# Kernel optimization log

Measured on AMD Instinct MI355X. Metric: run time of the kernel, lower is better.

Reference implementation:

```python
import jax, jax.numpy as jnp
import numpy as np

N_PTS0 = 32   # sample points per line
N_PTS1 = 8    # after 1d max-pool (kernel 4)
DIM_LOI = 128
DIM_FC = 1024
TOPK = 300
H = W = 128
L = 10000
C_FEAT = 256


def setup_inputs() -> dict:
    key = jax.random.key(0)
    ks = jax.random.split(key, 8)
    f32 = jnp.float32
    return {
        'output': jax.random.normal(ks[0], (1, 9, H, W), f32),
        'features': jax.random.normal(ks[1], (1, C_FEAT, H, W), f32),
        'lines_pred': jax.random.uniform(ks[2], (L, 4), f32, 0.0, W - 1.0),
        'fc1_w': jax.random.normal(ks[3], (DIM_LOI, C_FEAT), f32) * 0.05,
        'fc1_b': jnp.zeros((DIM_LOI,), f32),
        'w1': jax.random.normal(ks[4], (DIM_FC, DIM_LOI * N_PTS1), f32) * 0.02,
        'b1': jnp.zeros((DIM_FC,), f32),
        'w2': jax.random.normal(ks[5], (DIM_FC, DIM_FC), f32) * 0.02,
        'b2': jnp.zeros((DIM_FC,), f32),
        'w3': jax.random.normal(ks[6], (1, DIM_FC), f32) * 0.02,
        'b3': jnp.zeros((1,), f32),
    }


def _nms(a):
    # a: [H, W]; 3x3 max-pool NMS, keep only local maxima
    ap = jax.lax.reduce_window(a[None, None], -jnp.inf, jax.lax.max,
                               (1, 1, 3, 3), (1, 1, 1, 1), 'SAME')[0, 0]
    return a * (a == ap).astype(a.dtype)


def _pooling(loi, lines, w1, b1, w2, b2, w3, b3):
    # loi: [D, H, W]; lines: [L, 4]
    h, w = loi.shape[1], loi.shape[2]
    tspan = jnp.linspace(0.0, 1.0, N_PTS0)[None, None, :]          # [1,1,P]
    U, V = lines[:, :2], lines[:, 2:]
    pts = U[:, :, None] * tspan + V[:, :, None] * (1.0 - tspan) - 0.5  # [L,2,P]
    pts = jnp.transpose(pts, (0, 2, 1)).reshape(-1, 2)              # [L*P,2]
    px, py = pts[:, 0], pts[:, 1]
    px0 = jnp.clip(jnp.floor(px), 0, w - 1)
    py0 = jnp.clip(jnp.floor(py), 0, h - 1)
    px1 = jnp.clip(px0 + 1, 0, w - 1)
    py1 = jnp.clip(py0 + 1, 0, h - 1)
    ix0, iy0 = px0.astype(jnp.int32), py0.astype(jnp.int32)
    ix1, iy1 = px1.astype(jnp.int32), py1.astype(jnp.int32)
    xp = (loi[:, iy0, ix0] * (py1 - py) * (px1 - px)
          + loi[:, iy1, ix0] * (py - py0) * (px1 - px)
          + loi[:, iy0, ix1] * (py1 - py) * (px - px0)
          + loi[:, iy1, ix1] * (py - py0) * (px - px0))              # [D, L*P]
    xp = jnp.transpose(xp.reshape(DIM_LOI, -1, N_PTS0), (1, 0, 2))  # [L,D,P]
    k = N_PTS0 // N_PTS1
    xp = xp.reshape(xp.shape[0], DIM_LOI, N_PTS1, k).max(-1)        # maxpool1d
    feat = xp.reshape(-1, DIM_LOI * N_PTS1)                         # [L, D*P1]
    hid = jax.nn.relu(feat @ w1.T + b1)
    hid = jax.nn.relu(hid @ w2.T + b2)
    return (hid @ w3.T + b3).ravel()                                # logits [L]


def reference(output, features, lines_pred, fc1_w, fc1_b, w1, b1, w2, b2, w3, b3):
    height, width = output.shape[2], output.shape[3]
    # head decode
    jloc = jax.nn.softmax(output[0, 5:7], axis=0)[1]      # [H,W]
    joff = jax.nn.sigmoid(output[0, 7:9]) - 0.5           # [2,H,W]
    # NMS + top-k junction extraction
    jflat = _nms(jloc).reshape(-1)
    jscores, index = jax.lax.top_k(jflat, TOPK)
    joff_f = joff.reshape(2, -1)
    y = (index // width).astype(jnp.float32) + joff_f[1, index] + 0.5
    x = (index % width).astype(jnp.float32) + joff_f[0, index] + 0.5
    juncs = jnp.stack((x, y), axis=1)                     # [K,2]
    # pairwise endpoint-to-junction matching
    d1 = jnp.sum((lines_pred[None, :, :2] - juncs[:, None]) ** 2, -1)  # [K,L]
    d2 = jnp.sum((lines_pred[None, :, 2:] - juncs[:, None]) ** 2, -1)
    idx1 = jnp.argmin(d1, axis=0)
    idx2 = jnp.argmin(d2, axis=0)
    imin = jnp.minimum(idx1, idx2)
    imax = jnp.maximum(idx1, idx2)
    keep = imin < imax                                    # degenerate-line mask
    lines_adj = jnp.concatenate((juncs[imin], juncs[imax]), axis=1)  # [L,4]
    # 1x1 conv LOI features + bilinear line sampling + MLP verification
    loi = jnp.einsum('chw,dc->dhw', features[0], fc1_w) + fc1_b[:, None, None]
    logits = _pooling(loi, lines_adj, w1, b1, w2, b2, w3, b3)
    line_scores = jax.nn.sigmoid(logits) * keep.astype(logits.dtype)
    return line_scores, lines_adj, juncs, jscores
```

## Files before the change

### kernel.cpp

```cpp
#include <hip/hip_runtime.h>
#include <stdint.h>

#define HW      16384
#define WIDTH   128
#define NTOPK   300
#define NLINES  10000
#define MPAD2   10240

typedef unsigned short u16;
typedef unsigned int   u32;
typedef unsigned long long u64;
typedef __bf16 bf16x8 __attribute__((ext_vector_type(8)));
typedef float  f32x4  __attribute__((ext_vector_type(4)));

__device__ __forceinline__ u16 f2bf(float f) {
  u32 x = __builtin_bit_cast(u32, f);
  x += 0x7FFFu + ((x >> 16) & 1u);
  return (u16)(x >> 16);
}
__device__ __forceinline__ float bf2f(u32 u) {
  return __builtin_bit_cast(float, u << 16);
}
__device__ __forceinline__ void gload_lds16(void* lds, const void* g) {
  __builtin_amdgcn_global_load_lds(
      (const __attribute__((address_space(1))) void*)g,
      (__attribute__((address_space(3))) void*)lds, 16, 0, 0);
}

#define CF asm volatile("" ::: "memory")
#define BAR do { CF; __builtin_amdgcn_s_barrier(); CF; } while (0)
#define VM4 asm volatile("s_waitcnt vmcnt(4)" ::: "memory")
#define VM0 asm volatile("s_waitcnt vmcnt(0)" ::: "memory")

__global__ __launch_bounds__(1024) void k_topk(const float* __restrict__ out9,
                                               float* __restrict__ juncs_ws,
                                               float* __restrict__ out_juncs,
                                               float* __restrict__ out_jsc) {
  __shared__ float sig[HW];
  __shared__ u64 keys[4096];
  __shared__ int cnt;
  int t = threadIdx.x;
  if (t == 0) cnt = 0;
  for (int i = t; i < HW; i += 1024)
    sig[i] = 1.f / (1.f + expf(out9[5 * HW + i] - out9[6 * HW + i]));
  __syncthreads();
  for (int i = t; i < HW; i += 1024) {
    int x = i & (WIDTH - 1), y = i >> 7;
    float a = sig[i], m = a;
    for (int dy = -1; dy <= 1; ++dy) {
      int yy = y + dy;
      if (yy < 0 || yy >= WIDTH) continue;
      for (int dx = -1; dx <= 1; ++dx) {
        int xx = x + dx;
        if (xx < 0 || xx >= WIDTH) continue;
        m = fmaxf(m, sig[yy * WIDTH + xx]);
      }
    }
    if (a == m) {
      int pos = atomicAdd(&cnt, 1);
      if (pos < 4096)
        keys[pos] = ((u64)__builtin_bit_cast(u32, a) << 32) | (u32)(0xFFFFFFFFu - (u32)i);
    }
  }
  __syncthreads();
  int c = cnt < 4096 ? cnt : 4096;
  int n = (c <= 2048) ? 2048 : 4096;
  for (int i = t; i < n; i += 1024)
    if (i >= c) keys[i] = 0ull;
  __syncthreads();
  for (int k = 2; k <= n; k <<= 1) {
    for (int j = k >> 1; j > 0; j >>= 1) {
      for (int u = t; u < (n >> 1); u += 1024) {
        int i  = ((u & ~(j - 1)) << 1) | (u & (j - 1));
        int p  = i | j;
        u64 a = keys[i], b = keys[p];
        bool dir = (i & k) == 0;
        if ((a < b) == dir) { keys[i] = b; keys[p] = a; }
      }
      __syncthreads();
    }
  }
  if (t < NTOPK) {
    u64 key = keys[t];
    u32 vb  = (u32)(key >> 32);
    int idx = (int)(0xFFFFFFFFu - (u32)(key & 0xFFFFFFFFu));
    float ox = 1.f / (1.f + expf(-out9[7 * HW + idx])) - 0.5f;
    float oy = 1.f / (1.f + expf(-out9[8 * HW + idx])) - 0.5f;
    float x = (float)(idx & (WIDTH - 1)) + ox + 0.5f;
    float y = (float)(idx >> 7)          + oy + 0.5f;
    juncs_ws[2 * t] = x; juncs_ws[2 * t + 1] = y;
    out_juncs[2 * t] = x; out_juncs[2 * t + 1] = y;
    out_jsc[t] = __builtin_bit_cast(float, vb);
  }
}

__device__ __forceinline__ void acc8(uint4 r, float wg, float* a) {
  a[0] += bf2f(r.x & 0xffffu) * wg; a[1] += bf2f(r.x >> 16) * wg;
  a[2] += bf2f(r.y & 0xffffu) * wg; a[3] += bf2f(r.y >> 16) * wg;
  a[4] += bf2f(r.z & 0xffffu) * wg; a[5] += bf2f(r.z >> 16) * wg;
  a[6] += bf2f(r.w & 0xffffu) * wg; a[7] += bf2f(r.w >> 16) * wg;
}
__global__ __launch_bounds__(256) void k_minterp(const float* __restrict__ juncs,
                                                 const float* __restrict__ lines_pred,
                                                 const u16* __restrict__ loib,
                                                 float* __restrict__ lines_adj,
                                                 float* __restrict__ keepf,
                                                 u16* __restrict__ feat) {
  __shared__ float jl[2 * NTOPK];
  __shared__ u16 outb[4][8][128];
  int t = threadIdx.x;
  for (int i = t; i < 2 * NTOPK; i += 256) jl[i] = juncs[i];
  __syncthreads();
  int w = t >> 6, lane = t & 63;
  int l = blockIdx.x * 4 + w;
  float lx1 = lines_pred[l * 4 + 0], ly1 = lines_pred[l * 4 + 1];
  float lx2 = lines_pred[l * 4 + 2], ly2 = lines_pred[l * 4 + 3];
  float b1 = __builtin_inff(), b2 = __builtin_inff();
  int i1 = 0, i2 = 0;
  for (int j = lane; j < NTOPK; j += 64) {
    float jx = jl[2 * j], jy = jl[2 * j + 1];
    float dx = __fsub_rn(lx1, jx), dy = __fsub_rn(ly1, jy);
    float d  = __fadd_rn(__fmul_rn(dx, dx), __fmul_rn(dy, dy));
    if (d < b1) { b1 = d; i1 = j; }
    dx = __fsub_rn(lx2, jx); dy = __fsub_rn(ly2, jy);
    d  = __fadd_rn(__fmul_rn(dx, dx), __fmul_rn(dy, dy));
    if (d < b2) { b2 = d; i2 = j; }
  }
#pragma unroll
  for (int off = 1; off < 64; off <<= 1) {
    float d_o = __shfl_xor(b1, off, 64); int i_o = __shfl_xor(i1, off, 64);
    if (d_o < b1 || (d_o == b1 && i_o < i1)) { b1 = d_o; i1 = i_o; }
    d_o = __shfl_xor(b2, off, 64); i_o = __shfl_xor(i2, off, 64);
    if (d_o < b2 || (d_o == b2 && i_o < i2)) { b2 = d_o; i2 = i_o; }
  }
  int imin = i1 < i2 ? i1 : i2;
  int imax = i1 < i2 ? i2 : i1;
  float ux = jl[2 * imin], uy = jl[2 * imin + 1];
  float vx = jl[2 * imax], vy = jl[2 * imax + 1];
  if (lane == 0) {
    lines_adj[l * 4 + 0] = ux;
    lines_adj[l * 4 + 1] = uy;
    lines_adj[l * 4 + 2] = vx;
    lines_adj[l * 4 + 3] = vy;
    keepf[l] = (imin < imax) ? 1.f : 0.f;
  }
  int q = lane >> 4, chgrp = lane & 15, co = chgrp * 8;
#pragma unroll
  for (int s = 0; s < 8; ++s) {
    int p = s * 4 + q;
    float tt = (float)p / 31.f;
    float px = ux * tt + vx * (1.f - tt) - 0.5f;
    float py = uy * tt + vy * (1.f - tt) - 0.5f;
    float px0 = fminf(fmaxf(floorf(px), 0.f), 127.f);
    float py0 = fminf(fmaxf(floorf(py), 0.f), 127.f);
    float px1 = fminf(px0 + 1.f, 127.f);
    float py1 = fminf(py0 + 1.f, 127.f);
    int ix0 = (int)px0, iy0 = (int)py0, ix1 = (int)px1, iy1 = (int)py1;
    float wy1 = py1 - py, wy0 = py - py0, wx1 = px1 - px, wx0 = px - px0;
    uint4 v00 = *(const uint4*)&loib[(iy0 * WIDTH + ix0) * 128 + co];
    uint4 v10 = *(const uint4*)&loib[(iy1 * WIDTH + ix0) * 128 + co];
    uint4 v01 = *(const uint4*)&loib[(iy0 * WIDTH + ix1) * 128 + co];
    uint4 v11 = *(const uint4*)&loib[(iy1 * WIDTH + ix1) * 128 + co];
    float a[8];
#pragma unroll
    for (int cc = 0; cc < 8; ++cc) a[cc] = 0.f;
    acc8(v00, wy1 * wx1, a);
    acc8(v10, wy0 * wx1, a);
    acc8(v01, wy1 * wx0, a);
    acc8(v11, wy0 * wx0, a);
#pragma unroll
    for (int cc = 0; cc < 8; ++cc) {
      float v = fmaxf(a[cc], __shfl_xor(a[cc], 16, 64));
      v = fmaxf(v, __shfl_xor(v, 32, 64));
      a[cc] = v;
    }
    if (q == 0) {
      uint4 pk;
      pk.x = (u32)f2bf(a[0]) | ((u32)f2bf(a[1]) << 16);
      pk.y = (u32)f2bf(a[2]) | ((u32)f2bf(a[3]) << 16);
      pk.z = (u32)f2bf(a[4]) | ((u32)f2bf(a[5]) << 16);
      pk.w = (u32)f2bf(a[6]) | ((u32)f2bf(a[7]) << 16);
      *(uint4*)&outb[w][s][co] = pk;
    }
  }
  __syncthreads();
#pragma unroll
  for (int cc = 0; cc < 2; ++cc) {
    int ch = lane * 2 + cc;
    uint4 pk;
    pk.x = (u32)outb[w][0][ch] | ((u32)outb[w][1][ch] << 16);
    pk.y = (u32)outb[w][2][ch] | ((u32)outb[w][3][ch] << 16);
    pk.z = (u32)outb[w][4][ch] | ((u32)outb[w][5][ch] << 16);
    pk.w = (u32)outb[w][6][ch] | ((u32)outb[w][7][ch] << 16);
    *(uint4*)&feat[(size_t)l * 1024 + ch * 8] = pk;
  }
}

__global__ __launch_bounds__(256) void k_transp(const float* __restrict__ features,
                                                u16* __restrict__ featT) {
  __shared__ float tile[64][65];
  int t = threadIdx.x;
  int p0 = blockIdx.x * 64, c0 = blockIdx.y * 64;
#pragma unroll
  for (int i = 0; i < 4; ++i) {
    int lin = i * 256 + t;
    int c = lin >> 4, p4 = (lin & 15) * 4;
    float4 v = *(const float4*)&features[(size_t)(c0 + c) * HW + p0 + p4];
    tile[c][p4 + 0] = v.x; tile[c][p4 + 1] = v.y;
    tile[c][p4 + 2] = v.z; tile[c][p4 + 3] = v.w;
  }
  __syncthreads();
#pragma unroll
  for (int i = 0; i < 2; ++i) {
    int lin = i * 256 + t;
    int p = lin >> 3, c8 = (lin & 7) * 8;
    uint4 pk;
    pk.x = (u32)f2bf(tile[c8 + 0][p]) | ((u32)f2bf(tile[c8 + 1][p]) << 16);
    pk.y = (u32)f2bf(tile[c8 + 2][p]) | ((u32)f2bf(tile[c8 + 3][p]) << 16);
    pk.z = (u32)f2bf(tile[c8 + 4][p]) | ((u32)f2bf(tile[c8 + 5][p]) << 16);
    pk.w = (u32)f2bf(tile[c8 + 6][p]) | ((u32)f2bf(tile[c8 + 7][p]) << 16);
    *(uint4*)&featT[(size_t)(p0 + p) * 256 + c0 + c8] = pk;
  }
}

__global__ __launch_bounds__(256) void k_cvt3(const float* __restrict__ w1,
                                              const float* __restrict__ w2,
                                              const float* __restrict__ fc1,
                                              u16* __restrict__ d1,
                                              u16* __restrict__ d2,
                                              u16* __restrict__ d3) {
  int b = blockIdx.x;
  const float* s; u16* d; int base;
  if (b < 1024)      { s = w1;  d = d1; base = b * 1024; }
  else if (b < 2048) { s = w2;  d = d2; base = (b - 1024) * 1024; }
  else               { s = fc1; d = d3; base = (b - 2048) * 1024; }
  int i = base + threadIdx.x * 4;
  float4 v = *(const float4*)&s[i];
  uint2 pk;
  pk.x = (u32)f2bf(v.x) | ((u32)f2bf(v.y) << 16);
  pk.y = (u32)f2bf(v.z) | ((u32)f2bf(v.w) << 16);
  *(uint2*)&d[i] = pk;
}

template <int RELU>
__global__ __launch_bounds__(256) void k_gemm128(const u16* __restrict__ A,
                                                 const u16* __restrict__ B,
                                                 const float* __restrict__ bias,
                                                 u16* __restrict__ C,
                                                 int M, int N, int K) {
  __shared__ u16 Alds[128 * 32];
  __shared__ u16 Blds[128 * 32];
  int nwg = gridDim.x * gridDim.y;
  int bid = blockIdx.y * gridDim.x + blockIdx.x;
  int cpx = nwg >> 3;
  int key = (bid & 7) * cpx + (bid >> 3);
  int bx = key / gridDim.y;
  int by = key % gridDim.y;
  int t = threadIdx.x;
  int tm0 = bx * 128;
  int tn0 = by * 128;
  int lane = t & 63, wid = t >> 6;
  int wr = wid >> 1, wc = wid & 1;
  f32x4 acc[4][4] = {};
  int arow = t >> 2, apos = (t & 3) * 8;
  const u16* Abase = A + (size_t)tm0 * K;
  const u16* Bbase = B + (size_t)tn0 * K;
  int r = lane & 15, ks = (lane >> 4) * 8;
  for (int k0 = 0; k0 < K; k0 += 32) {
    gload_lds16(&Alds[(size_t)t * 8],         Abase + (size_t)arow * K + k0 + apos);
    gload_lds16(&Alds[(size_t)(t + 256) * 8], Abase + (size_t)(arow + 64) * K + k0 + apos);
    gload_lds16(&Blds[(size_t)t * 8],         Bbase + (size_t)arow * K + k0 + apos);
    gload_lds16(&Blds[(size_t)(t + 256) * 8], Bbase + (size_t)(arow + 64) * K + k0 + apos);
    __syncthreads();
    bf16x8 af[4], bfr[4];
#pragma unroll
    for (int i = 0; i < 4; ++i) {
      af[i]  = *(const bf16x8*)&Alds[(wr * 64 + i * 16 + r) * 32 + ks];
      bfr[i] = *(const bf16x8*)&Blds[(wc * 64 + i * 16 + r) * 32 + ks];
    }
#pragma unroll
    for (int mi = 0; mi < 4; ++mi)
#pragma unroll
      for (int ni = 0; ni < 4; ++ni)
        acc[mi][ni] = __builtin_amdgcn_mfma_f32_16x16x32_bf16(af[mi], bfr[ni], acc[mi][ni], 0, 0, 0);
    __syncthreads();
  }
  int rsub = (lane >> 4) * 4, csub = lane & 15;
#pragma unroll
  for (int mi = 0; mi < 4; ++mi) {
#pragma unroll
    for (int ni = 0; ni < 4; ++ni) {
      int col = tn0 + wc * 64 + ni * 16 + csub;
      float bv = bias[col];
#pragma unroll
      for (int j = 0; j < 4; ++j) {
        int row = tm0 + wr * 64 + mi * 16 + rsub + j;
        float v = acc[mi][ni][j] + bv;
        if (RELU) v = fmaxf(v, 0.f);
        C[(size_t)row * N + col] = f2bf(v);
      }
    }
  }
}

__device__ __forceinline__ void stg256(u16* S, int ldsbase, const u16* Xb,
                                       size_t sbase, int K, int kt, int h, int dbase) {
  gload_lds16(&S[ldsbase + h * 8192 + dbase],
              Xb + sbase + (size_t)(h * 128) * K + kt * 64);
  gload_lds16(&S[ldsbase + h * 8192 + 4096 + dbase],
              Xb + sbase + (size_t)(h * 128 + 64) * K + kt * 64);
}
template <int RH>
__device__ __forceinline__ void lda4(bf16x8 (*dst)[2], const u16* Sa, int rowA,
                                     int kx0, int kx1) {
#pragma unroll
  for (int f = 0; f < 4; ++f) {
    const u16* p = Sa + rowA + (RH * 64 + f * 16) * 64;
    dst[f][0] = *(const bf16x8*)&p[kx0];
    dst[f][1] = *(const bf16x8*)&p[kx1];
  }
}
template <int CH>
__device__ __forceinline__ void ldb2(bf16x8 (*dst)[2], const u16* Sb, int rowB,
                                     int kx0, int kx1) {
#pragma unroll
  for (int cf = 0; cf < 2; ++cf) {
    const u16* p = Sb + rowB + (CH * 32 + cf * 16) * 64;
    dst[cf][0] = *(const bf16x8*)&p[kx0];
    dst[cf][1] = *(const bf16x8*)&p[kx1];
  }
}
template <int RH, int CH>
__device__ __forceinline__ void mm16(f32x4 (*acc)[4], bf16x8 (*af)[2], bf16x8 (*bf)[2]) {
  __builtin_amdgcn_s_setprio(1);
#pragma unroll
  for (int f = 0; f < 4; ++f)
#pragma unroll
    for (int cf = 0; cf < 2; ++cf) {
      f32x4 a = acc[RH * 4 + f][CH * 2 + cf];
      a = __builtin_amdgcn_mfma_f32_16x16x32_bf16(af[f][0], bf[cf][0], a, 0, 0, 0);
      a = __builtin_amdgcn_mfma_f32_16x16x32_bf16(af[f][1], bf[cf][1], a, 0, 0, 0);
      acc[RH * 4 + f][CH * 2 + cf] = a;
    }
  __builtin_amdgcn_s_setprio(0);
}

template <int RELU, int HEAD>
__global__ __launch_bounds__(512, 2) void k_gemm256(const u16* __restrict__ A,
                                                    const u16* __restrict__ B,
                                                    const float* __restrict__ bias,
                                                    u16* __restrict__ C,
                                                    const float* __restrict__ w3,
                                                    float* __restrict__ partial,
                                                    int M, int N, int K) {
  __shared__ u16 S[65536];
  const int t = threadIdx.x, lane = t & 63, w = t >> 6;
  const int wm = w >> 2, wn = w & 3;
  int nwg = gridDim.x * gridDim.y;
  int bid = blockIdx.y * gridDim.x + blockIdx.x;
  int cpx = nwg >> 3;
  int key = (bid & 7) * cpx + (bid >> 3);
  int bx = key / gridDim.y, by = key % gridDim.y;
  const u16* Ab = A + (size_t)(bx * 256) * K;
  const u16* Bb = B + (size_t)(by * 256) * K;
  const int srow = w * 8 + (lane >> 3);
  const size_t sbase = (size_t)srow * K + ((lane & 7) ^ (lane >> 3)) * 8;
  const int dbase = w * 512 + lane * 8;
  const int l15 = lane & 15, hi = lane >> 4, l7 = lane & 7;
  const int rowA = (wm * 128 + l15) * 64;
  const int rowB = (wn * 64 + l15) * 64;
  const int kx0 = ((0 + hi) ^ l7) * 8;
  const int kx1 = ((4 + hi) ^ l7) * 8;
  const u16* SA0 = S;
  const u16* SA1 = S + 16384;
  const u16* SB0 = S + 32768;
  const u16* SB1 = S + 49152;
  f32x4 acc[8][4] = {};
  bf16x8 af0[4][2], af1[4][2], bf0[2][2], bf1[2][2];
  const int NI = K >> 7;
  stg256(S, 0,     Ab, sbase, K, 0, 0, dbase);
  stg256(S, 0,     Ab, sbase, K, 0, 1, dbase);
  stg256(S, 32768, Bb, sbase, K, 0, 0, dbase);
  stg256(S, 32768, Bb, sbase, K, 0, 1, dbase);
  stg256(S, 16384, Ab, sbase, K, 1, 0, dbase);
  stg256(S, 16384, Ab, sbase, K, 1, 1, dbase);
  VM4; BAR;
  for (int j = 0; j < NI - 1; ++j) {
    int kt = 2 * j;
    lda4<0>(af0, SA0, rowA, kx0, kx1);
    ldb2<0>(bf0, SB0, rowB, kx0, kx1);
    stg256(S, 49152, Bb, sbase, K, kt + 1, 0, dbase);
    BAR; mm16<0, 0>(acc, af0, bf0); BAR;
    lda4<1>(af1, SA0, rowA, kx0, kx1);
    stg256(S, 49152, Bb, sbase, K, kt + 1, 1, dbase);
    BAR; mm16<1, 0>(acc, af1, bf0); BAR;
    ldb2<1>(bf1, SB0, rowB, kx0, kx1);
    stg256(S, 0, Ab, sbase, K, kt + 2, 0, dbase);
    BAR; mm16<0, 1>(acc, af0, bf1); BAR;
    stg256(S, 0, Ab, sbase, K, kt + 2, 1, dbase);
    VM4;
    BAR; mm16<1, 1>(acc, af1, bf1); BAR;
    lda4<0>(af0, SA1, rowA, kx0, kx1);
    ldb2<0>(bf0, SB1, rowB, kx0, kx1);
    stg256(S, 32768, Bb, sbase, K, kt + 2, 0, dbase);
    BAR; mm16<0, 0>(acc, af0, bf0); BAR;
    lda4<1>(af1, SA1, rowA, kx0, kx1);
    stg256(S, 32768, Bb, sbase, K, kt + 2, 1, dbase);
    BAR; mm16<1, 0>(acc, af1, bf0); BAR;
    ldb2<1>(bf1, SB1, rowB, kx0, kx1);
    stg256(S, 16384, Ab, sbase, K, kt + 3, 0, dbase);
    BAR; mm16<0, 1>(acc, af0, bf1); BAR;
    stg256(S, 16384, Ab, sbase, K, kt + 3, 1, dbase);
    VM4;
    BAR; mm16<1, 1>(acc, af1, bf1); BAR;
  }
  {
    int kt = 2 * (NI - 1);
    lda4<0>(af0, SA0, rowA, kx0, kx1);
    ldb2<0>(bf0, SB0, rowB, kx0, kx1);
    stg256(S, 49152, Bb, sbase, K, kt + 1, 0, dbase);
    BAR; mm16<0, 0>(acc, af0, bf0); BAR;
    lda4<1>(af1, SA0, rowA, kx0, kx1);
    stg256(S, 49152, Bb, sbase, K, kt + 1, 1, dbase);
    BAR; mm16<1, 0>(acc, af1, bf0); BAR;
    ldb2<1>(bf1, SB0, rowB, kx0, kx1);
    BAR; mm16<0, 1>(acc, af0, bf1); BAR;
    VM0;
    BAR; mm16<1, 1>(acc, af1, bf1); BAR;
    lda4<0>(af0, SA1, rowA, kx0, kx1);
    ldb2<0>(bf0, SB1, rowB, kx0, kx1);
    BAR; mm16<0, 0>(acc, af0, bf0); BAR;
    lda4<1>(af1, SA1, rowA, kx0, kx1);
    BAR; mm16<1, 0>(acc, af1, bf0); BAR;
    ldb2<1>(bf1, SB1, rowB, kx0, kx1);
    BAR; mm16<0, 1>(acc, af0, bf1); BAR;
    mm16<1, 1>(acc, af1, bf1);
  }
  int row0 = bx * 256 + wm * 128 + hi * 4;
  int col0 = by * 256 + wn * 64 + l15;
  if (HEAD == 0) {
#pragma unroll
    for (int f = 0; f < 8; ++f) {
#pragma unroll
      for (int cf = 0; cf < 4; ++cf) {
        float bv = bias[col0 + cf * 16];
#pragma unroll
        for (int jj = 0; jj < 4; ++jj) {
          float v = acc[f][cf][jj] + bv;
          if (RELU) v = fmaxf(v, 0.f);
          C[(size_t)(row0 + f * 16 + jj) * N + col0 + cf * 16] = f2bf(v);
        }
      }
    }
  } else {
    float bv[4], wv[4];
#pragma unroll
    for (int cf = 0; cf < 4; ++cf) {
      bv[cf] = bias[col0 + cf * 16];
      wv[cf] = w3[col0 + cf * 16];
    }
#pragma unroll
    for (int f = 0; f < 8; ++f) {
#pragma unroll
      for (int jj = 0; jj < 4; ++jj) {
        float p = 0.f;
#pragma unroll
        for (int cf = 0; cf < 4; ++cf) {
          float v = acc[f][cf][jj] + bv[cf];
          v = fmaxf(v, 0.f);
          p += v * wv[cf];
        }
        p += __shfl_xor(p, 1, 64);
        p += __shfl_xor(p, 2, 64);
        p += __shfl_xor(p, 4, 64);
        p += __shfl_xor(p, 8, 64);
        if (l15 == 0)
          partial[(size_t)(by * 4 + wn) * M + row0 + f * 16 + jj] = p;
      }
    }
  }
}

__global__ __launch_bounds__(256) void k_head2(const float* __restrict__ partial,
                                               const float* __restrict__ b3,
                                               const float* __restrict__ keepf,
                                               float* __restrict__ scores, int M) {
  int l = blockIdx.x * 256 + threadIdx.x;
  if (l >= NLINES) return;
  float s = 0.f;
#pragma unroll
  for (int i = 0; i < 16; ++i) s += partial[(size_t)i * M + l];
  float logit = s + b3[0];
  scores[l] = keepf[l] / (1.f + expf(-logit));
}

extern "C" void kernel_launch(void* const* d_in, const int* in_sizes, int n_in,
                              void* d_out, int out_size, void* d_ws, size_t ws_size,
                              hipStream_t stream) {
  const float* t_output   = (const float*)d_in[0];
  const float* t_features = (const float*)d_in[1];
  const float* t_lines    = (const float*)d_in[2];
  const float* t_fc1w     = (const float*)d_in[3];
  const float* t_fc1b     = (const float*)d_in[4];
  const float* t_w1       = (const float*)d_in[5];
  const float* t_b1       = (const float*)d_in[6];
  const float* t_w2       = (const float*)d_in[7];
  const float* t_b2       = (const float*)d_in[8];
  const float* t_w3       = (const float*)d_in[9];
  const float* t_b3       = (const float*)d_in[10];

  char* w = (char*)d_ws;
  u16*   loib  = (u16*)w;
  float* juncs = (float*)(w + 4194304);
  float* keepf = juncs + 1024;
  u16* fc1wb = (u16*)(keepf + 10240);
  u16* w1b  = fc1wb + 32768;
  u16* w2b  = w1b + 1048576;
  u16* feat = w2b + 1048576;
  u16* hid1 = feat + (size_t)MPAD2 * 1024;
  float* partial = (float*)(hid1 + (size_t)MPAD2 * 1024);
  u16* featT = hid1;

  float* out_scores = (float*)d_out;
  float* out_ladj   = out_scores + NLINES;
  float* out_juncs  = out_scores + 50000;
  float* out_jsc    = out_scores + 50600;

  k_cvt3<<<2080, 256, 0, stream>>>(t_w1, t_w2, t_fc1w, w1b, w2b, fc1wb);
  k_topk<<<1, 1024, 0, stream>>>(t_output, juncs, out_juncs, out_jsc);
  k_transp<<<dim3(256, 4), 256, 0, stream>>>(t_features, featT);
  k_gemm128<0><<<dim3(128, 1), 256, 0, stream>>>(featT, fc1wb, t_fc1b, loib, HW, 128, 256);
  k_minterp<<<2500, 256, 0, stream>>>(juncs, t_lines, loib, out_ladj, keepf, feat);
  k_gemm256<1, 0><<<dim3(40, 4), 512, 0, stream>>>(feat, w1b, t_b1, hid1,
                                                   nullptr, nullptr, MPAD2, 1024, 1024);
  k_gemm256<0, 1><<<dim3(40, 4), 512, 0, stream>>>(hid1, w2b, t_b2, nullptr,
                                                   t_w3, partial, MPAD2, 1024, 1024);
  k_head2<<<40, 256, 0, stream>>>(partial, t_b3, keepf, out_scores, MPAD2);
}
```

Measured before the change: 165.1 us.

## Merge front-end kernels and parallelize NMS across blocks before single-block top-k sort

Replaces the separate weight-conversion, single-block top-k, transpose and LOI GEMM launches with two kernels. The first runs tiled NMS across 64 blocks alongside the feature transpose and weight conversion. The second runs the top-k sort in one block while the other blocks compute the 1x1-conv GEMM concurrently. This cuts launch count and takes the serial sigmoid/NMS pass off the single 1024-thread block, at the cost of a workspace round trip for candidate keys and a sort using only 256 threads.

```diff
diff --git a/kernel.cpp b/kernel.cpp
--- a/kernel.cpp
+++ b/kernel.cpp
@@ -32,65 +32,193 @@
 #define VM4 asm volatile("s_waitcnt vmcnt(4)" ::: "memory")
 #define VM0 asm volatile("s_waitcnt vmcnt(0)" ::: "memory")
 
-__global__ __launch_bounds__(1024) void k_topk(const float* __restrict__ out9,
-                                               float* __restrict__ juncs_ws,
-                                               float* __restrict__ out_juncs,
-                                               float* __restrict__ out_jsc) {
-  __shared__ float sig[HW];
-  __shared__ u64 keys[4096];
-  __shared__ int cnt;
+__global__ __launch_bounds__(256) void k_front1(const float* __restrict__ out9,
+                                                const float* __restrict__ features,
+                                                const float* __restrict__ w1,
+                                                const float* __restrict__ w2,
+                                                const float* __restrict__ fc1,
+                                                u16* __restrict__ featT,
+                                                u16* __restrict__ w1b,
+                                                u16* __restrict__ w2b,
+                                                u16* __restrict__ fc1wb,
+                                                u64* __restrict__ wkeys,
+                                                int* __restrict__ bcnt) {
+  __shared__ float sm[64 * 65];
+  __shared__ int lcnt;
+  int b = blockIdx.x, t = threadIdx.x;
+  if (b < 64) {
+    float (*jl)[18] = (float(*)[18])sm;
+    if (t == 0) lcnt = 0;
+    int bx = b & 7, by = b >> 3;
+    int gx0 = bx * 16 - 1, gy0 = by * 16 - 1;
+    for (int lin = t; lin < 324; lin += 256) {
+      int lx = lin % 18, ly = lin / 18;
+      int gx = gx0 + lx, gy = gy0 + ly;
+      float v = -__builtin_inff();
+      if (gx >= 0 && gx < WIDTH && gy >= 0 && gy < WIDTH) {
+        int i = gy * WIDTH + gx;
+        v = 1.f / (1.f + expf(out9[5 * HW + i] - out9[6 * HW + i]));
+      }
+      jl[ly][lx] = v;
+    }
+    __syncthreads();
+    int tx = t & 15, ty = t >> 4;
+    float a = jl[ty + 1][tx + 1], m = a;
+#pragma unroll
+    for (int dy = 0; dy < 3; ++dy)
+#pragma unroll
+      for (int dx = 0; dx < 3; ++dx)
+        m = fmaxf(m, jl[ty + dy][tx + dx]);
+    if (a == m) {
+      int pos = atomicAdd(&lcnt, 1);
+      int i = (by * 16 + ty) * WIDTH + bx * 16 + tx;
+      wkeys[b * 256 + pos] =
+          ((u64)__builtin_bit_cast(u32, a) << 32) | (u32)(0xFFFFFFFFu - (u32)i);
+    }
+    __syncthreads();
+    if (t == 0) bcnt[b] = lcnt;
+  } else if (b < 1088) {
+    float (*tile)[65] = (float(*)[65])sm;
+    int bb = b - 64;
+    int p0 = (bb & 255) * 64, c0 = (bb >> 8) * 64;
+#pragma unroll
+    for (int i = 0; i < 4; ++i) {
+      int lin = i * 256 + t;
+      int c = lin >> 4, p4 = (lin & 15) * 4;
+      float4 v = *(const float4*)&features[(size_t)(c0 + c) * HW + p0 + p4];
+      tile[c][p4 + 0] = v.x; tile[c][p4 + 1] = v.y;
+      tile[c][p4 + 2] = v.z; tile[c][p4 + 3] = v.w;
+    }
+    __syncthreads();
+#pragma unroll
+    for (int i = 0; i < 2; ++i) {
+      int lin = i * 256 + t;
+      int p = lin >> 3, c8 = (lin & 7) * 8;
+      uint4 pk;
+      pk.x = (u32)f2bf(tile[c8 + 0][p]) | ((u32)f2bf(tile[c8 + 1][p]) << 16);
+      pk.y = (u32)f2bf(tile[c8 + 2][p]) | ((u32)f2bf(tile[c8 + 3][p]) << 16);
+      pk.z = (u32)f2bf(tile[c8 + 4][p]) | ((u32)f2bf(tile[c8 + 5][p]) << 16);
+      pk.w = (u32)f2bf(tile[c8 + 6][p]) | ((u32)f2bf(tile[c8 + 7][p]) << 16);
+      *(uint4*)&featT[(size_t)(p0 + p) * 256 + c0 + c8] = pk;
+    }
+  } else {
+    int idx = b - 1088;
+    const float* s; u16* d; int base;
+    if (idx < 256)      { s = w1;  d = w1b;  base = idx * 4096; }
+    else if (idx < 512) { s = w2;  d = w2b;  base = (idx - 256) * 4096; }
+    else                { s = fc1; d = fc1wb; base = (idx - 512) * 4096; }
+#pragma unroll
+    for (int r = 0; r < 4; ++r) {
+      int i = base + r * 1024 + t * 4;
+      float4 v = *(const float4*)&s[i];
+      uint2 pk;
+      pk.x = (u32)f2bf(v.x) | ((u32)f2bf(v.y) << 16);
+      pk.y = (u32)f2bf(v.z) | ((u32)f2bf(v.w) << 16);
+      *(uint2*)&d[i] = pk;
+    }
+  }
+}
+
+__global__ __launch_bounds__(256) void k_front2(const u64* __restrict__ wkeys,
+                                                const int* __restrict__ bcnt,
+                                                const float* __restrict__ out9,
+                                                float* __restrict__ juncs_ws,
+                                                float* __restrict__ out_juncs,
+                                                float* __restrict__ out_jsc,
+                                                const u16* __restrict__ featT,
+                                                const u16* __restrict__ fc1wb,
+                                                const float* __restrict__ fc1b,
+                                                u16* __restrict__ loib) {
+  __shared__ u64 smem[4096];
+  __shared__ int lcnt;
   int t = threadIdx.x;
-  if (t == 0) cnt = 0;
-  for (int i = t; i < HW; i += 1024)
-    sig[i] = 1.f / (1.f + expf(out9[5 * HW + i] - out9[6 * HW + i]));
-  __syncthreads();
-  for (int i = t; i < HW; i += 1024) {
-    int x = i & (WIDTH - 1), y = i >> 7;
-    float a = sig[i], m = a;
-    for (int dy = -1; dy <= 1; ++dy) {
-      int yy = y + dy;
-      if (yy < 0 || yy >= WIDTH) continue;
-      for (int dx = -1; dx <= 1; ++dx) {
-        int xx = x + dx;
-        if (xx < 0 || xx >= WIDTH) continue;
-        m = fmaxf(m, sig[yy * WIDTH + xx]);
-      }
-    }
-    if (a == m) {
-      int pos = atomicAdd(&cnt, 1);
-      if (pos < 4096)
-        keys[pos] = ((u64)__builtin_bit_cast(u32, a) << 32) | (u32)(0xFFFFFFFFu - (u32)i);
-    }
-  }
-  __syncthreads();
-  int c = cnt < 4096 ? cnt : 4096;
-  int n = (c <= 2048) ? 2048 : 4096;
-  for (int i = t; i < n; i += 1024)
-    if (i >= c) keys[i] = 0ull;
-  __syncthreads();
-  for (int k = 2; k <= n; k <<= 1) {
-    for (int j = k >> 1; j > 0; j >>= 1) {
-      for (int u = t; u < (n >> 1); u += 1024) {
-        int i  = ((u & ~(j - 1)) << 1) | (u & (j - 1));
-        int p  = i | j;
-        u64 a = keys[i], b = keys[p];
-        bool dir = (i & k) == 0;
-        if ((a < b) == dir) { keys[i] = b; keys[p] = a; }
-      }
+  if (blockIdx.x == 0) {
+    u64* keys = smem;
+    if (t == 0) lcnt = 0;
+    __syncthreads();
+    for (int j = t; j < 64 * 256; j += 256) {
+      int bb = j >> 8, ii = j & 255;
+      if (ii < bcnt[bb]) {
+        int pos = atomicAdd(&lcnt, 1);
+        if (pos < 4096) keys[pos] = wkeys[j];
+      }
+    }
+    __syncthreads();
+    int c = lcnt < 4096 ? lcnt : 4096;
+    int n = (c <= 2048) ? 2048 : 4096;
+    for (int i = t; i < n; i += 256)
+      if (i >= c) keys[i] = 0ull;
+    __syncthreads();
+    for (int k = 2; k <= n; k <<= 1) {
+      for (int j = k >> 1; j > 0; j >>= 1) {
+        for (int u = t; u < (n >> 1); u += 256) {
+          int i  = ((u & ~(j - 1)) << 1) | (u & (j - 1));
+          int p  = i | j;
+          u64 a = keys[i], bkey = keys[p];
+          bool dir = (i & k) == 0;
+          if ((a < bkey) == dir) { keys[i] = bkey; keys[p] = a; }
+        }
+        __syncthreads();
+      }
+    }
+    for (int i = t; i < NTOPK; i += 256) {
+      u64 key = keys[i];
+      u32 vb  = (u32)(key >> 32);
+      int idx = (int)(0xFFFFFFFFu - (u32)(key & 0xFFFFFFFFu));
+      float ox = 1.f / (1.f + expf(-out9[7 * HW + idx])) - 0.5f;
+      float oy = 1.f / (1.f + expf(-out9[8 * HW + idx])) - 0.5f;
+      float x = (float)(idx & (WIDTH - 1)) + ox + 0.5f;
+      float y = (float)(idx >> 7)          + oy + 0.5f;
+      juncs_ws[2 * i] = x; juncs_ws[2 * i + 1] = y;
+      out_juncs[2 * i] = x; out_juncs[2 * i + 1] = y;
+      out_jsc[i] = __builtin_bit_cast(float, vb);
+    }
+  } else {
+    u16* Alds = (u16*)smem;
+    u16* Blds = (u16*)smem + 4096;
+    const int K = 256, N = 128;
+    int bid = blockIdx.x - 1;
+    int key = (bid & 7) * 16 + (bid >> 3);
+    int tm0 = key * 128;
+    int lane = t & 63, wid = t >> 6;
+    int wr = wid >> 1, wc = wid & 1;
+    f32x4 acc[4][4] = {};
+    int arow = t >> 2, apos = (t & 3) * 8;
+    const u16* Abase = featT + (size_t)tm0 * K;
+    int r = lane & 15, ks = (lane >> 4) * 8;
+    for (int k0 = 0; k0 < K; k0 += 32) {
+      gload_lds16(&Alds[(size_t)t * 8],         Abase + (size_t)arow * K + k0 + apos);
+      gload_lds16(&Alds[(size_t)(t + 256) * 8], Abase + (size_t)(arow + 64) * K + k0 + apos);
+      gload_lds16(&Blds[(size_t)t * 8],         fc1wb + (size_t)arow * K + k0 + apos);
+      gload_lds16(&Blds[(size_t)(t + 256) * 8], fc1wb + (size_t)(arow + 64) * K + k0 + apos);
       __syncthreads();
-    }
-  }
-  if (t < NTOPK) {
-    u64 key = keys[t];
-    u32 vb  = (u32)(key >> 32);
-    int idx = (int)(0xFFFFFFFFu - (u32)(key & 0xFFFFFFFFu));
-    float ox = 1.f / (1.f + expf(-out9[7 * HW + idx])) - 0.5f;
-    float oy = 1.f / (1.f + expf(-out9[8 * HW + idx])) - 0.5f;
-    float x = (float)(idx & (WIDTH - 1)) + ox + 0.5f;
-    float y = (float)(idx >> 7)          + oy + 0.5f;
-    juncs_ws[2 * t] = x; juncs_ws[2 * t + 1] = y;
-    out_juncs[2 * t] = x; out_juncs[2 * t + 1] = y;
-    out_jsc[t] = __builtin_bit_cast(float, vb);
+      bf16x8 af[4], bfr[4];
+#pragma unroll
+      for (int i = 0; i < 4; ++i) {
+        af[i]  = *(const bf16x8*)&Alds[(wr * 64 + i * 16 + r) * 32 + ks];
+        bfr[i] = *(const bf16x8*)&Blds[(wc * 64 + i * 16 + r) * 32 + ks];
+      }
+#pragma unroll
+      for (int mi = 0; mi < 4; ++mi)
+#pragma unroll
+        for (int ni = 0; ni < 4; ++ni)
+          acc[mi][ni] = __builtin_amdgcn_mfma_f32_16x16x32_bf16(af[mi], bfr[ni], acc[mi][ni], 0, 0, 0);
+      __syncthreads();
+    }
+    int rsub = (lane >> 4) * 4, csub = lane & 15;
+#pragma unroll
+    for (int mi = 0; mi < 4; ++mi) {
+#pragma unroll
+      for (int ni = 0; ni < 4; ++ni) {
+        int col = wc * 64 + ni * 16 + csub;
+        float bv = fc1b[col];
+#pragma unroll
+        for (int j = 0; j < 4; ++j) {
+          int row = tm0 + wr * 64 + mi * 16 + rsub + j;
+          loib[(size_t)row * N + col] = f2bf(acc[mi][ni][j] + bv);
+        }
+      }
+    }
   }
 }
 
@@ -193,113 +321,6 @@
     pk.z = (u32)outb[w][4][ch] | ((u32)outb[w][5][ch] << 16);
     pk.w = (u32)outb[w][6][ch] | ((u32)outb[w][7][ch] << 16);
     *(uint4*)&feat[(size_t)l * 1024 + ch * 8] = pk;
-  }
-}
-
-__global__ __launch_bounds__(256) void k_transp(const float* __restrict__ features,
-                                                u16* __restrict__ featT) {
-  __shared__ float tile[64][65];
-  int t = threadIdx.x;
-  int p0 = blockIdx.x * 64, c0 = blockIdx.y * 64;
-#pragma unroll
-  for (int i = 0; i < 4; ++i) {
-    int lin = i * 256 + t;
-    int c = lin >> 4, p4 = (lin & 15) * 4;
-    float4 v = *(const float4*)&features[(size_t)(c0 + c) * HW + p0 + p4];
-    tile[c][p4 + 0] = v.x; tile[c][p4 + 1] = v.y;
-    tile[c][p4 + 2] = v.z; tile[c][p4 + 3] = v.w;
-  }
-  __syncthreads();
-#pragma unroll
-  for (int i = 0; i < 2; ++i) {
-    int lin = i * 256 + t;
-    int p = lin >> 3, c8 = (lin & 7) * 8;
-    uint4 pk;
-    pk.x = (u32)f2bf(tile[c8 + 0][p]) | ((u32)f2bf(tile[c8 + 1][p]) << 16);
-    pk.y = (u32)f2bf(tile[c8 + 2][p]) | ((u32)f2bf(tile[c8 + 3][p]) << 16);
-    pk.z = (u32)f2bf(tile[c8 + 4][p]) | ((u32)f2bf(tile[c8 + 5][p]) << 16);
-    pk.w = (u32)f2bf(tile[c8 + 6][p]) | ((u32)f2bf(tile[c8 + 7][p]) << 16);
-    *(uint4*)&featT[(size_t)(p0 + p) * 256 + c0 + c8] = pk;
-  }
-}
-
-__global__ __launch_bounds__(256) void k_cvt3(const float* __restrict__ w1,
-                                              const float* __restrict__ w2,
-                                              const float* __restrict__ fc1,
-                                              u16* __restrict__ d1,
-                                              u16* __restrict__ d2,
-                                              u16* __restrict__ d3) {
-  int b = blockIdx.x;
-  const float* s; u16* d; int base;
-  if (b < 1024)      { s = w1;  d = d1; base = b * 1024; }
-  else if (b < 2048) { s = w2;  d = d2; base = (b - 1024) * 1024; }
-  else               { s = fc1; d = d3; base = (b - 2048) * 1024; }
-  int i = base + threadIdx.x * 4;
-  float4 v = *(const float4*)&s[i];
-  uint2 pk;
-  pk.x = (u32)f2bf(v.x) | ((u32)f2bf(v.y) << 16);
-  pk.y = (u32)f2bf(v.z) | ((u32)f2bf(v.w) << 16);
-  *(uint2*)&d[i] = pk;
-}
-
-template <int RELU>
-__global__ __launch_bounds__(256) void k_gemm128(const u16* __restrict__ A,
-                                                 const u16* __restrict__ B,
-                                                 const float* __restrict__ bias,
-                                                 u16* __restrict__ C,
-                                                 int M, int N, int K) {
-  __shared__ u16 Alds[128 * 32];
-  __shared__ u16 Blds[128 * 32];
-  int nwg = gridDim.x * gridDim.y;
-  int bid = blockIdx.y * gridDim.x + blockIdx.x;
-  int cpx = nwg >> 3;
-  int key = (bid & 7) * cpx + (bid >> 3);
-  int bx = key / gridDim.y;
-  int by = key % gridDim.y;
-  int t = threadIdx.x;
-  int tm0 = bx * 128;
-  int tn0 = by * 128;
-  int lane = t & 63, wid = t >> 6;
-  int wr = wid >> 1, wc = wid & 1;
-  f32x4 acc[4][4] = {};
-  int arow = t >> 2, apos = (t & 3) * 8;
-  const u16* Abase = A + (size_t)tm0 * K;
-  const u16* Bbase = B + (size_t)tn0 * K;
-  int r = lane & 15, ks = (lane >> 4) * 8;
-  for (int k0 = 0; k0 < K; k0 += 32) {
-    gload_lds16(&Alds[(size_t)t * 8],         Abase + (size_t)arow * K + k0 + apos);
-    gload_lds16(&Alds[(size_t)(t + 256) * 8], Abase + (size_t)(arow + 64) * K + k0 + apos);
-    gload_lds16(&Blds[(size_t)t * 8],         Bbase + (size_t)arow * K + k0 + apos);
-    gload_lds16(&Blds[(size_t)(t + 256) * 8], Bbase + (size_t)(arow + 64) * K + k0 + apos);
-    __syncthreads();
-    bf16x8 af[4], bfr[4];
-#pragma unroll
-    for (int i = 0; i < 4; ++i) {
-      af[i]  = *(const bf16x8*)&Alds[(wr * 64 + i * 16 + r) * 32 + ks];
-      bfr[i] = *(const bf16x8*)&Blds[(wc * 64 + i * 16 + r) * 32 + ks];
-    }
-#pragma unroll
-    for (int mi = 0; mi < 4; ++mi)
-#pragma unroll
-      for (int ni = 0; ni < 4; ++ni)
-        acc[mi][ni] = __builtin_amdgcn_mfma_f32_16x16x32_bf16(af[mi], bfr[ni], acc[mi][ni], 0, 0, 0);
-    __syncthreads();
-  }
-  int rsub = (lane >> 4) * 4, csub = lane & 15;
-#pragma unroll
-  for (int mi = 0; mi < 4; ++mi) {
-#pragma unroll
-    for (int ni = 0; ni < 4; ++ni) {
-      int col = tn0 + wc * 64 + ni * 16 + csub;
-      float bv = bias[col];
-#pragma unroll
-      for (int j = 0; j < 4; ++j) {
-        int row = tm0 + wr * 64 + mi * 16 + rsub + j;
-        float v = acc[mi][ni][j] + bv;
-        if (RELU) v = fmaxf(v, 0.f);
-        C[(size_t)row * N + col] = f2bf(v);
-      }
-    }
   }
 }
 
@@ -513,7 +534,9 @@
   u16*   loib  = (u16*)w;
   float* juncs = (float*)(w + 4194304);
   float* keepf = juncs + 1024;
-  u16* fc1wb = (u16*)(keepf + 10240);
+  int*   bcnt  = (int*)(keepf + 10240);
+  u64*   wkeys = (u64*)(bcnt + 256);
+  u16* fc1wb = (u16*)(wkeys + 16384);
   u16* w1b  = fc1wb + 32768;
   u16* w2b  = w1b + 1048576;
   u16* feat = w2b + 1048576;
@@ -526,10 +549,11 @@
   float* out_juncs  = out_scores + 50000;
   float* out_jsc    = out_scores + 50600;
 
-  k_cvt3<<<2080, 256, 0, stream>>>(t_w1, t_w2, t_fc1w, w1b, w2b, fc1wb);
-  k_topk<<<1, 1024, 0, stream>>>(t_output, juncs, out_juncs, out_jsc);
-  k_transp<<<dim3(256, 4), 256, 0, stream>>>(t_features, featT);
-  k_gemm128<0><<<dim3(128, 1), 256, 0, stream>>>(featT, fc1wb, t_fc1b, loib, HW, 128, 256);
+  k_front1<<<1608, 256, 0, stream>>>(t_output, t_features, t_w1, t_w2, t_fc1w,
+                                     featT, w1b, w2b, fc1wb, wkeys, bcnt);
+  k_front2<<<129, 256, 0, stream>>>(wkeys, bcnt, t_output,
+                                    juncs, out_juncs, out_jsc,
+                                    featT, fc1wb, t_fc1b, loib);
   k_minterp<<<2500, 256, 0, stream>>>(juncs, t_lines, loib, out_ladj, keepf, feat);
   k_gemm256<1, 0><<<dim3(40, 4), 512, 0, stream>>>(feat, w1b, t_b1, hid1,
                                                    nullptr, nullptr, MPAD2, 1024, 1024);
```

Result: slower. 180.6 us (+9.4%).
